# Optimization experiments

Hardware: AMD Instinct MI355X
Metric: run time of the kernel (lower is better)

## Reference

```python
import jax, jax.numpy as jnp
import numpy as np

N_NODES = 100000
N_EDGES = 1600000
IN_CH, GCN_CH, OUT_CH = 64, 64, 32


def gcn_conv(x, W, b, row, col, ew):
    """PyG GCNConv: normalize=True, add_self_loops=True (weight 1.0)."""
    N = x.shape[0]
    deg = jax.ops.segment_sum(ew, col, num_segments=N) + 1.0  # self-loop weight 1
    dis = jax.lax.rsqrt(deg)                                   # deg >= 1
    norm = dis[row] * ew * dis[col]                            # [E]
    xw = x @ W                                                 # [N, C_out]
    agg = jax.ops.segment_sum(norm[:, None] * xw[row], col, num_segments=N)
    # self-loop contribution: dis[i] * 1 * dis[i] * xw[i]
    return agg + (dis * dis)[:, None] * xw + b


def setup_inputs() -> dict:
    key = jax.random.key(0)
    ks = jax.random.split(key, 9)
    x = jax.random.normal(ks[0], (N_NODES, IN_CH), dtype=jnp.float32)
    edge_index = jax.random.randint(ks[1], (2, N_EDGES), 0, N_NODES, dtype=jnp.int64)
    edge_weight = jax.random.uniform(ks[2], (N_EDGES,), dtype=jnp.float32)
    s1 = 1.0 / np.sqrt(IN_CH)
    s2 = 1.0 / np.sqrt(GCN_CH)
    W1 = jax.random.uniform(ks[3], (IN_CH, GCN_CH), jnp.float32, -s1, s1)
    b1 = jnp.zeros((GCN_CH,), jnp.float32)
    W2 = jax.random.uniform(ks[4], (GCN_CH, GCN_CH), jnp.float32, -s2, s2)
    b2 = jnp.zeros((GCN_CH,), jnp.float32)
    Wout = jax.random.uniform(ks[5], (GCN_CH, OUT_CH), jnp.float32, -s2, s2)
    bout = jax.random.uniform(ks[6], (OUT_CH,), jnp.float32, -s2, s2)
    return {"x": x, "edge_index": edge_index, "edge_weight": edge_weight,
            "W1": W1, "b1": b1, "W2": W2, "b2": b2, "Wout": Wout, "bout": bout}


def reference(x, edge_index, edge_weight, W1, b1, W2, b2, Wout, bout):
    row, col = edge_index[0], edge_index[1]
    h = jax.nn.relu(gcn_conv(x, W1, b1, row, col, edge_weight))
    h = jax.nn.relu(gcn_conv(h, W2, b2, row, col, edge_weight))
    return jnp.tanh(h @ Wout + bout)
```

## Files before the change

### kernel.cpp

```cpp
#include <hip/hip_runtime.h>
#include <hip/hip_fp16.h>
#include <math.h>

#define N_NODES 100000
#define N_EDGES 1600000
#define IN_CH   64
#define GCN_CH  64
#define OUT_CH  32
#define MAXDEG  48

#define EW_SCALE  32768.0f
#define EW_INV    (1.0f / 32768.0f)

#define BSHIFT   7
#define NBUCK    1024
#define NBUCK_USED ((N_NODES + 127) / 128)
#define EPB      4096
#define NBLK     ((N_EDGES + EPB - 1) / EPB)
#define HIST_TOT (NBUCK * NBLK)
#define NCHUNK   (HIST_TOT / 1024)
#define GEMMB    ((N_NODES + 63) / 64)

typedef _Float16 f16x2 __attribute__((ext_vector_type(2)));

__device__ inline float fdot2(__half2 a, __half2 b, float c) {
    f16x2 av, bv;
    __builtin_memcpy(&av, &a, 4);
    __builtin_memcpy(&bv, &b, 4);
    return __builtin_amdgcn_fdot2(av, bv, c, false);
}

__global__ void hist_kernel(const int* __restrict__ col, unsigned* __restrict__ hist_g) {
    __shared__ unsigned sh[NBUCK];
    int blk = blockIdx.x;
    for (int i = threadIdx.x; i < NBUCK; i += 1024) sh[i] = 0;
    __syncthreads();
    int base = blk * EPB;
    int lim  = min(EPB, N_EDGES - base);
    for (int i = threadIdx.x; i < lim; i += 1024)
        atomicAdd(&sh[(unsigned)col[base + i] >> BSHIFT], 1u);
    __syncthreads();
    for (int b = threadIdx.x; b < NBUCK; b += 1024)
        hist_g[(size_t)b * NBLK + blk] = sh[b];
}

__global__ void scan1_kernel(const unsigned* __restrict__ in, unsigned* __restrict__ outp,
                             unsigned* __restrict__ blockSums) {
    __shared__ unsigned sdata[256];
    int t = threadIdx.x;
    int base = blockIdx.x * 1024 + t * 4;
    unsigned v[4];
    unsigned sum = 0;
#pragma unroll
    for (int i = 0; i < 4; ++i) { v[i] = in[base + i]; sum += v[i]; }
    sdata[t] = sum;
    __syncthreads();
    for (int off = 1; off < 256; off <<= 1) {
        unsigned x = (t >= off) ? sdata[t - off] : 0;
        __syncthreads();
        sdata[t] += x;
        __syncthreads();
    }
    unsigned excl = sdata[t] - sum;
    if (t == 255) blockSums[blockIdx.x] = sdata[t];
    unsigned run = excl;
#pragma unroll
    for (int i = 0; i < 4; ++i) { outp[base + i] = run; run += v[i]; }
}

__device__ inline void chunk_scan(const unsigned* __restrict__ bsum, unsigned* cb,
                                  int t) {
    if (t < 512) cb[t] = (t < NCHUNK) ? bsum[t] : 0u;
    __syncthreads();
    for (int off = 1; off < 512; off <<= 1) {
        unsigned x = 0;
        if (t < 512 && t >= off) x = cb[t - off];
        __syncthreads();
        if (t < 512) cb[t] += x;
        __syncthreads();
    }
}

__global__ void scatter_gemm_kernel(const int* __restrict__ row, const int* __restrict__ col,
                                    const float* __restrict__ ew,
                                    const unsigned* __restrict__ scanned,
                                    const unsigned* __restrict__ blockSums,
                                    unsigned long long* __restrict__ srt,
                                    const float* __restrict__ X, const float* __restrict__ W,
                                    __half* __restrict__ Y) {
    __shared__ unsigned cur[NBUCK];
    __shared__ unsigned cb[512];
    __shared__ float4   Ws[64][16];
    int t = threadIdx.x;
    int bid = blockIdx.x;

    if (bid < NBLK) {
        chunk_scan(blockSums, cb, t);
        int blk = bid;
        for (int b = t; b < NBUCK; b += 1024) {
            size_t hidx = (size_t)b * NBLK + blk;
            unsigned chunk = (unsigned)(hidx >> 10);
            cur[b] = scanned[hidx] + (chunk ? cb[chunk - 1] : 0u);
        }
        __syncthreads();
        int base = blk * EPB;
        int lim  = min(EPB, N_EDGES - base);
        for (int i = t; i < lim; i += 1024) {
            int e = base + i;
            unsigned c = (unsigned)col[e];
            unsigned r = (unsigned)row[e];
            float    w = ew[e];
            unsigned u15 = min((unsigned)(w * EW_SCALE + 0.5f), 32767u);
            unsigned rec = (r << 15) | u15;
            unsigned pos = atomicAdd(&cur[c >> BSHIFT], 1u);
            srt[pos] = ((unsigned long long)c << 32) | rec;
        }
    } else {
        ((float4*)Ws)[t] = ((const float4*)W)[t];
        __syncthreads();
        int gb  = bid - NBLK;
        int q   = t & 15;
        int sub = t >> 4;
        int rw  = gb * 64 + sub;
        if (rw >= N_NODES) return;
        const float4* xr = (const float4*)(X + (size_t)rw * 64);
        float4 acc = {0.f, 0.f, 0.f, 0.f};
#pragma unroll
        for (int k4 = 0; k4 < 16; ++k4) {
            float4 xv = xr[k4];
#pragma unroll
            for (int j = 0; j < 4; ++j) {
                float xs = (j == 0) ? xv.x : (j == 1) ? xv.y : (j == 2) ? xv.z : xv.w;
                float4 wv = Ws[k4 * 4 + j][q];
                acc.x = fmaf(xs, wv.x, acc.x);
                acc.y = fmaf(xs, wv.y, acc.y);
                acc.z = fmaf(xs, wv.z, acc.z);
                acc.w = fmaf(xs, wv.w, acc.w);
            }
        }
        union { __half2 h[2]; float2 f; } u;
        u.h[0] = __floats2half2_rn(acc.x, acc.y);
        u.h[1] = __floats2half2_rn(acc.z, acc.w);
        *(float2*)(Y + (size_t)rw * 64 + q * 4) = u.f;
    }
}

__global__ void ell_fill_kernel(const unsigned* __restrict__ scanned,
                                const unsigned* __restrict__ blockSums,
                                const unsigned long long* __restrict__ srt,
                                unsigned* __restrict__ ell,
                                unsigned* __restrict__ deg_arr, float* __restrict__ dis) {
    __shared__ unsigned cb[512];
    __shared__ unsigned cur[128];
    __shared__ float    wsum[128];
    int t = threadIdx.x;
    chunk_scan(blockSums, cb, t);
    if (t < 128) { cur[t] = 0; wsum[t] = 0.f; }
    __syncthreads();
    int b = blockIdx.x;
    size_t h0 = (size_t)b * NBLK;
    size_t h1 = (size_t)(b + 1) * NBLK;
    unsigned c0 = (unsigned)(h0 >> 10), c1 = (unsigned)(h1 >> 10);
    unsigned start = scanned[h0] + (c0 ? cb[c0 - 1] : 0u);
    unsigned end   = (b + 1 < NBUCK) ? (scanned[h1] + (c1 ? cb[c1 - 1] : 0u))
                                     : (unsigned)N_EDGES;
    for (unsigned i = start + t; i < end; i += 512) {
        unsigned long long v = srt[i];
        unsigned c   = (unsigned)(v >> 32);
        unsigned rec = (unsigned)v;
        unsigned cl  = c & 127u;
        unsigned k   = atomicAdd(&cur[cl], 1u);
        if (k < MAXDEG) ell[(size_t)c * MAXDEG + k] = rec;
        atomicAdd(&wsum[cl], (float)(rec & 32767u) * EW_INV);
    }
    __syncthreads();
    if (t < 128) {
        int c = b * 128 + t;
        if (c < N_NODES) {
            deg_arr[c] = min(cur[t], (unsigned)MAXDEG);
            dis[c]     = rsqrtf(wsum[t] + 1.0f);
        }
    }
}

__global__ void gemm64h_f16_kernel(const __half* __restrict__ X, const float* __restrict__ W,
                                   __half* __restrict__ Y, int nrows) {
    __shared__ float4 Ws[64][16];
    int t = threadIdx.x;
    for (int i = t; i < 64 * 16; i += 256)
        ((float4*)Ws)[i] = ((const float4*)W)[i];
    __syncthreads();

    int q   = t & 15;
    int sub = t >> 4;
    int row = blockIdx.x * 16 + sub;
    if (row >= nrows) return;
    const float4* xr = (const float4*)(X + (size_t)row * 64);
    float4 acc = {0.f, 0.f, 0.f, 0.f};
#pragma unroll
    for (int k8 = 0; k8 < 8; ++k8) {
        float4 raw = xr[k8];
        const __half2* hp = (const __half2*)&raw;
#pragma unroll
        for (int j = 0; j < 4; ++j) {
            float xs0 = __low2float(hp[j]);
            float xs1 = __high2float(hp[j]);
            float4 w0 = Ws[k8 * 8 + 2 * j][q];
            float4 w1 = Ws[k8 * 8 + 2 * j + 1][q];
            acc.x = fmaf(xs0, w0.x, acc.x); acc.y = fmaf(xs0, w0.y, acc.y);
            acc.z = fmaf(xs0, w0.z, acc.z); acc.w = fmaf(xs0, w0.w, acc.w);
            acc.x = fmaf(xs1, w1.x, acc.x); acc.y = fmaf(xs1, w1.y, acc.y);
            acc.z = fmaf(xs1, w1.z, acc.z); acc.w = fmaf(xs1, w1.w, acc.w);
        }
    }
    union { __half2 h[2]; float2 f; } u;
    u.h[0] = __floats2half2_rn(acc.x, acc.y);
    u.h[1] = __floats2half2_rn(acc.z, acc.w);
    *(float2*)(Y + (size_t)row * 64 + q * 4) = u.f;
}

__device__ inline void make_h_raw(const float* acc, float4 xraw,
                                  const float* b, int q, float dd, float* h) {
    const __half2* hp = (const __half2*)&xraw;
    float4 b0 = *(const float4*)(b + q * 8);
    float4 b1 = *(const float4*)(b + q * 8 + 4);
    float xs[8] = {__low2float(hp[0]), __high2float(hp[0]),
                   __low2float(hp[1]), __high2float(hp[1]),
                   __low2float(hp[2]), __high2float(hp[2]),
                   __low2float(hp[3]), __high2float(hp[3])};
    float bb[8] = {b0.x, b0.y, b0.z, b0.w, b1.x, b1.y, b1.z, b1.w};
#pragma unroll
    for (int i = 0; i < 8; ++i)
        h[i] = fmaxf(fmaf(dd, xs[i], acc[i]) + bb[i], 0.f);
}

__device__ inline void fma_pk(float4 raw, __half2 nv, __half2* acc) {
    const __half2* ha = (const __half2*)&raw;
    acc[0] = __hfma2(nv, ha[0], acc[0]);
    acc[1] = __hfma2(nv, ha[1], acc[1]);
    acc[2] = __hfma2(nv, ha[2], acc[2]);
    acc[3] = __hfma2(nv, ha[3], acc[3]);
}

__device__ inline void gather_core(int node, int lane,
                                   const unsigned* __restrict__ deg_arr,
                                   const unsigned* __restrict__ ell,
                                   const __half* __restrict__ XWh,
                                   const float* __restrict__ dis,
                                   float& dc_out, float4& xself, float* accf) {
    int half = lane >> 5;
    int l    = lane & 31;
    int g    = l >> 3;
    int q    = l & 7;
    int base = half << 5;

    int deg = (int)deg_arr[node];
    const unsigned* erow = ell + (size_t)node * MAXDEG;
    unsigned rec1 = (l < deg) ? erow[l] : 0u;
    unsigned rec2 = (l < 16 && 32 + l < deg) ? erow[32 + l] : 0u;
    float dc = dis[node];
    dc_out = dc;

    int   src1 = (int)(rec1 >> 15);
    float nv1  = dis[src1] * ((float)(rec1 & 32767u) * EW_INV) * dc;
    int   src2 = (int)(rec2 >> 15);
    float nv2  = dis[src2] * ((float)(rec2 & 32767u) * EW_INV) * dc;
    __half2 t1 = __float2half2_rn(nv1), t2 = __float2half2_rn(nv2);
    int nv1pk, nv2pk;
    __builtin_memcpy(&nv1pk, &t1, 4);
    __builtin_memcpy(&nv2pk, &t2, 4);

    xself = *(const float4*)(XWh + (size_t)node * 64 + q * 8);

    int dmax = max(deg, __shfl_xor(deg, 32, 64));

    __half2 acc[4] = {__float2half2_rn(0.f), __float2half2_rn(0.f),
                      __float2half2_rn(0.f), __float2half2_rn(0.f)};
    int s1 = min(dmax, 32);
    for (int s = 0; s < s1; s += 16) {
        int srcA  = __shfl(src1,  base + s + g, 64);
        int nvA_i = __shfl(nv1pk, base + s + g, 64);
        int srcB  = __shfl(src1,  base + s + 4 + g, 64);
        int nvB_i = __shfl(nv1pk, base + s + 4 + g, 64);
        int srcC  = __shfl(src1,  base + s + 8 + g, 64);
        int nvC_i = __shfl(nv1pk, base + s + 8 + g, 64);
        int srcD  = __shfl(src1,  base + s + 12 + g, 64);
        int nvD_i = __shfl(nv1pk, base + s + 12 + g, 64);
        float4 rawA = *(const float4*)(XWh + (size_t)srcA * 64 + q * 8);
        float4 rawB = *(const float4*)(XWh + (size_t)srcB * 64 + q * 8);
        float4 rawC = *(const float4*)(XWh + (size_t)srcC * 64 + q * 8);
        float4 rawD = *(const float4*)(XWh + (size_t)srcD * 64 + q * 8);
        __half2 nvA, nvB, nvC, nvD;
        __builtin_memcpy(&nvA, &nvA_i, 4);
        __builtin_memcpy(&nvB, &nvB_i, 4);
        __builtin_memcpy(&nvC, &nvC_i, 4);
        __builtin_memcpy(&nvD, &nvD_i, 4);
        fma_pk(rawA, nvA, acc);
        fma_pk(rawB, nvB, acc);
        fma_pk(rawC, nvC, acc);
        fma_pk(rawD, nvD, acc);
    }
    if (dmax > 32) {
        for (int s = 32; s < dmax; s += 4) {
            int srcB  = __shfl(src2,  base + (s - 32) + g, 64);
            int nvB_i = __shfl(nv2pk, base + (s - 32) + g, 64);
            float4 raw = *(const float4*)(XWh + (size_t)srcB * 64 + q * 8);
            __half2 nvB; __builtin_memcpy(&nvB, &nvB_i, 4);
            fma_pk(raw, nvB, acc);
        }
    }
#pragma unroll
    for (int m = 8; m <= 16; m <<= 1) {
#pragma unroll
        for (int i = 0; i < 4; ++i) {
            int ai; __builtin_memcpy(&ai, &acc[i], 4);
            int bi = __shfl_xor(ai, m, 64);
            __half2 bh; __builtin_memcpy(&bh, &bi, 4);
            acc[i] = __hadd2(acc[i], bh);
        }
    }
#pragma unroll
    for (int i = 0; i < 4; ++i) {
        accf[2 * i]     = __low2float(acc[i]);
        accf[2 * i + 1] = __high2float(acc[i]);
    }
}

__global__ void gather_h_kernel(const unsigned* __restrict__ deg_arr,
                                const unsigned* __restrict__ ell,
                                const __half* __restrict__ XWh,
                                const float* __restrict__ dis, const float* __restrict__ b,
                                __half* __restrict__ H) {
    int lane = threadIdx.x & 63;
    int node = blockIdx.x * 16 + (threadIdx.x >> 6) * 2 + (lane >> 5);
    int l = lane & 31;
    int q = l & 7;

    float dc; float4 xself; float accf[8];
    gather_core(node, lane, deg_arr, ell, XWh, dis, dc, xself, accf);

    if ((l >> 3) == 0) {
        float h[8];
        make_h_raw(accf, xself, b, q, dc * dc, h);
        union { __half2 hh[4]; float4 f; } u;
        u.hh[0] = __floats2half2_rn(h[0], h[1]);
        u.hh[1] = __floats2half2_rn(h[2], h[3]);
        u.hh[2] = __floats2half2_rn(h[4], h[5]);
        u.hh[3] = __floats2half2_rn(h[6], h[7]);
        *(float4*)(H + (size_t)node * 64 + q * 8) = u.f;
    }
}

__global__ void gather_out_kernel(const unsigned* __restrict__ deg_arr,
                                  const unsigned* __restrict__ ell,
                                  const __half* __restrict__ XWh,
                                  const float* __restrict__ dis, const float* __restrict__ b,
                                  const float* __restrict__ Wout, const float* __restrict__ bout,
                                  float* __restrict__ OUT) {
    __shared__ __half2 Ws2[32][32];
    {
        for (int idx = threadIdx.x; idx < 32 * 32; idx += (int)blockDim.x) {
            int kp = idx >> 5, j = idx & 31;
            Ws2[kp][j] = __floats2half2_rn(Wout[(2 * kp) * OUT_CH + j],
                                           Wout[(2 * kp + 1) * OUT_CH + j]);
        }
        __syncthreads();
    }

    int lane = threadIdx.x & 63;
    int node = blockIdx.x * 16 + (threadIdx.x >> 6) * 2 + (lane >> 5);
    int half = lane >> 5;
    int l = lane & 31;
    int q = l & 7;
    int base = half << 5;

    float dc; float4 xself; float accf[8];
    gather_core(node, lane, deg_arr, ell, XWh, dis, dc, xself, accf);

    float h[8];
    make_h_raw(accf, xself, b, q, dc * dc, h);

    int hpk[4];
#pragma unroll
    for (int i = 0; i < 4; ++i) {
        __half2 t2 = __floats2half2_rn(h[2 * i], h[2 * i + 1]);
        __builtin_memcpy(&hpk[i], &t2, 4);
    }
    float partial = 0.f;
#pragma unroll
    for (int kk = 0; kk < 32; ++kk) {
        int hv_i = __shfl(hpk[kk & 3], base + (kk >> 2), 64);
        __half2 hv; __builtin_memcpy(&hv, &hv_i, 4);
        partial = fdot2(hv, Ws2[kk][l], partial);
    }
    float v = partial + bout[l];
    float e = __expf(2.f * v);
    OUT[(size_t)node * OUT_CH + l] = 1.f - 2.f / (e + 1.f);
}

extern "C" void kernel_launch(void* const* d_in, const int* in_sizes, int n_in,
                              void* d_out, int out_size, void* d_ws, size_t ws_size,
                              hipStream_t stream) {
    const float* x     = (const float*)d_in[0];
    const int*   eidx  = (const int*)  d_in[1];
    const float* ew    = (const float*)d_in[2];
    const float* W1    = (const float*)d_in[3];
    const float* b1    = (const float*)d_in[4];
    const float* W2    = (const float*)d_in[5];
    const float* b2    = (const float*)d_in[6];
    const float* Wout  = (const float*)d_in[7];
    const float* bout  = (const float*)d_in[8];
    float*       out   = (float*)d_out;

    const int* row = eidx;
    const int* col = eidx + N_EDGES;

    char*  ws   = (char*)d_ws;
    size_t offs = 0;
    auto alloc = [&](size_t bytes) {
        char* p = ws + offs;
        offs += (bytes + 1023) & ~(size_t)1023;
        return p;
    };
    unsigned* hist_g    = (unsigned*)alloc((size_t)HIST_TOT * sizeof(unsigned));
    unsigned* scanned   = (unsigned*)alloc((size_t)HIST_TOT * sizeof(unsigned));
    unsigned* blockSums = (unsigned*)alloc((size_t)NCHUNK * sizeof(unsigned));
    unsigned long long* srt = (unsigned long long*)alloc((size_t)N_EDGES * 8);
    unsigned* deg_arr   = (unsigned*)alloc((size_t)N_NODES * sizeof(unsigned));
    float*    dis       = (float*)   alloc((size_t)N_NODES * sizeof(float));
    unsigned* ell       = (unsigned*)alloc((size_t)N_NODES * MAXDEG * sizeof(unsigned));
    __half*   xwh       = (__half*)  alloc((size_t)N_NODES * GCN_CH * sizeof(__half));
    __half*   hbuf      = (__half*)srt;

    const int BLK  = 256;
    const int BLKG = 512;
    const int gGemm   = (N_NODES + 15) / 16;
    const int gGather = N_NODES / 16;

    hist_kernel<<<NBLK, 1024, 0, stream>>>(col, hist_g);
    scan1_kernel<<<NCHUNK, 256, 0, stream>>>(hist_g, scanned, blockSums);
    scatter_gemm_kernel<<<NBLK + GEMMB, 1024, 0, stream>>>(row, col, ew, scanned,
                                                           blockSums, srt, x, W1, xwh);
    ell_fill_kernel<<<NBUCK_USED, 512, 0, stream>>>(scanned, blockSums, srt,
                                                    ell, deg_arr, dis);

    gather_h_kernel<<<gGather, BLKG, 0, stream>>>(deg_arr, ell, xwh, dis, b1, hbuf);

    gemm64h_f16_kernel<<<gGemm, BLK, 0, stream>>>(hbuf, W2, xwh, N_NODES);
    gather_out_kernel<<<gGather, BLKG, 0, stream>>>(deg_arr, ell, xwh, dis, b2,
                                                    Wout, bout, out);
}
```

Measured before the change: 156.2 us.

## Locally sort edges per block in LDS before coalesced global scatter

The scatter phase now counts bucket occupancy per block, scans those counts in shared memory, and places records into an LDS staging array grouped by bucket. It then writes them to global memory in bucket-contiguous order, so consecutive threads write neighbouring addresses instead of scattering randomly. The aim is better write coalescing to the sorted edge buffer. The cost is an extra 32KB of LDS, another atomic pass and extra barriers, which may lower occupancy for this kernel.

New measurement: 152.8 us, median of 2. -2.2%, faster.

```diff
diff --git a/kernel.cpp b/kernel.cpp
--- a/kernel.cpp
+++ b/kernel.cpp
@@ -88,32 +88,78 @@
                                     unsigned long long* __restrict__ srt,
                                     const float* __restrict__ X, const float* __restrict__ W,
                                     __half* __restrict__ Y) {
+    __shared__ unsigned cb[512];
     __shared__ unsigned cur[NBUCK];
-    __shared__ unsigned cb[512];
+    __shared__ unsigned lbase[NBUCK];
+    __shared__ unsigned lcur[NBUCK];
+    __shared__ unsigned wsum[16];
+    __shared__ unsigned long long lrec[EPB];
     __shared__ float4   Ws[64][16];
     int t = threadIdx.x;
     int bid = blockIdx.x;
 
     if (bid < NBLK) {
         chunk_scan(blockSums, cb, t);
-        int blk = bid;
-        for (int b = t; b < NBUCK; b += 1024) {
-            size_t hidx = (size_t)b * NBLK + blk;
-            unsigned chunk = (unsigned)(hidx >> 10);
-            cur[b] = scanned[hidx] + (chunk ? cb[chunk - 1] : 0u);
-        }
-        __syncthreads();
+        lcur[t] = 0;
+        __syncthreads();
+
+        int blk  = bid;
         int base = blk * EPB;
         int lim  = min(EPB, N_EDGES - base);
-        for (int i = t; i < lim; i += 1024) {
-            int e = base + i;
+
+        unsigned long long recs[4];
+        unsigned bks[4];
+#pragma unroll
+        for (int k = 0; k < 4; ++k) {
+            int i = t + k * 1024;
+            bool ok = i < lim;
+            int e = base + (ok ? i : 0);
             unsigned c = (unsigned)col[e];
             unsigned r = (unsigned)row[e];
             float    w = ew[e];
             unsigned u15 = min((unsigned)(w * EW_SCALE + 0.5f), 32767u);
-            unsigned rec = (r << 15) | u15;
-            unsigned pos = atomicAdd(&cur[c >> BSHIFT], 1u);
-            srt[pos] = ((unsigned long long)c << 32) | rec;
+            recs[k] = ((unsigned long long)c << 32) | ((r << 15) | u15);
+            bks[k]  = c >> BSHIFT;
+            if (ok) atomicAdd(&lcur[bks[k]], 1u);
+        }
+        __syncthreads();
+
+        {
+            unsigned v = lcur[t];
+            unsigned inc = v;
+#pragma unroll
+            for (int off = 1; off < 64; off <<= 1) {
+                unsigned u = __shfl_up(inc, off, 64);
+                if ((t & 63) >= off) inc += u;
+            }
+            if ((t & 63) == 63) wsum[t >> 6] = inc;
+            __syncthreads();
+            unsigned wprefix = 0;
+            int wid = t >> 6;
+            for (int wv = 0; wv < wid; ++wv) wprefix += wsum[wv];
+            lbase[t] = wprefix + inc - v;
+            size_t hidx = (size_t)t * NBLK + blk;
+            unsigned chunk = (unsigned)(hidx >> 10);
+            cur[t]  = scanned[hidx] + (chunk ? cb[chunk - 1] : 0u);
+            lcur[t] = lbase[t];
+        }
+        __syncthreads();
+
+#pragma unroll
+        for (int k = 0; k < 4; ++k) {
+            int i = t + k * 1024;
+            if (i < lim) {
+                unsigned p = atomicAdd(&lcur[bks[k]], 1u);
+                lrec[p] = recs[k];
+            }
+        }
+        __syncthreads();
+
+        for (int j = t; j < lim; j += 1024) {
+            unsigned long long v = lrec[j];
+            unsigned b = (unsigned)(v >> 32) >> BSHIFT;
+            unsigned gpos = cur[b] + ((unsigned)j - lbase[b]);
+            srt[gpos] = v;
         }
     } else {
         ((float4*)Ws)[t] = ((const float4*)W)[t];
```
